# Kernel optimization log

Measured on AMD Instinct MI355X. Metric: run time of the kernel, lower is better.

## Reference

```python
import jax, jax.numpy as jnp
import numpy as np

B, S, DM, H = 4, 2048, 512, 8
HD = DM // H


def setup_inputs() -> dict:
    key = jax.random.key(0)
    ks = jax.random.split(key, 12)
    x = jax.random.normal(ks[0], (B, S, DM), dtype=jnp.float32)
    # causal lower-triangular mask [B, S, S]
    mask = jnp.broadcast_to(jnp.tril(jnp.ones((S, S), dtype=jnp.int32)), (B, S, S))
    # sorted irregular day offsets (trading-day-like), in days
    days_offset = jnp.sort(
        jax.random.uniform(ks[1], (B, S), dtype=jnp.float32) * 3000.0, axis=-1
    )
    scale = 1.0 / np.sqrt(DM)
    Wq = jax.random.normal(ks[2], (DM, DM), dtype=jnp.float32) * scale
    bq = jnp.zeros((DM,), dtype=jnp.float32)
    Wk = jax.random.normal(ks[3], (DM, DM), dtype=jnp.float32) * scale
    bk = jnp.zeros((DM,), dtype=jnp.float32)
    Wv = jax.random.normal(ks[4], (DM, DM), dtype=jnp.float32) * scale
    bv = jnp.zeros((DM,), dtype=jnp.float32)
    Wo = jax.random.normal(ks[5], (DM, DM), dtype=jnp.float32) * scale
    bo = jnp.zeros((DM,), dtype=jnp.float32)
    decay_rate = jnp.float32(0.1)
    return {
        "x": x, "mask": mask, "days_offset": days_offset,
        "Wq": Wq, "bq": bq, "Wk": Wk, "bk": bk,
        "Wv": Wv, "bv": bv, "Wo": Wo, "bo": bo,
        "decay_rate": decay_rate,
    }


def reference(x, mask, days_offset, Wq, bq, Wk, bk, Wv, bv, Wo, bo, decay_rate):
    b, s, _ = x.shape
    # projections (torch Linear: x @ W.T + b), split heads -> [b, h, s, hd]
    def proj(W, bias):
        return (x @ W.T + bias).reshape(b, s, H, HD).transpose(0, 2, 1, 3)
    q, k, v = proj(Wq, bq), proj(Wk, bk), proj(Wv, bv)
    scores = jnp.einsum("bhqd,bhkd->bhqk", q, k) / jnp.sqrt(jnp.float32(HD))
    # temporal decay: exp(-rate * |t_i - t_j|), broadcast over heads
    dist = jnp.abs(days_offset[:, :, None] - days_offset[:, None, :])  # [b,s,s]
    decay = jnp.exp(-decay_rate * dist)
    scores = scores * decay[:, None, :, :]
    scores = jnp.where(mask[:, None, :, :] == 0, -jnp.inf, scores)
    attn = jax.nn.softmax(scores, axis=-1)  # dropout p=0 (eval)
    out = jnp.einsum("bhqk,bhkd->bhqd", attn, v)
    out = out.transpose(0, 2, 1, 3).reshape(b, s, DM)
    return out @ Wo.T + bo
```

## Files before the change

kernel.cpp:

```cpp
#include <hip/hip_runtime.h>
#include <hip/hip_fp16.h>


#define S_LEN 2048
#define DMODEL 512
#define NH 8
#define HD 64

typedef _Float16 half8 __attribute__((ext_vector_type(8)));
typedef _Float16 half4 __attribute__((ext_vector_type(4)));
typedef float floatx4 __attribute__((ext_vector_type(4)));

__device__ __forceinline__ void gload16(const _Float16* g, _Float16* l) {
    __builtin_amdgcn_global_load_lds(
        (const __attribute__((address_space(1))) void*)g,
        (__attribute__((address_space(3))) void*)l, 16, 0, 0);
}

__device__ __forceinline__ half8 cvt8(float4 a, float4 b) {
    half8 h;
    h[0] = (_Float16)a.x; h[1] = (_Float16)a.y; h[2] = (_Float16)a.z; h[3] = (_Float16)a.w;
    h[4] = (_Float16)b.x; h[5] = (_Float16)b.y; h[6] = (_Float16)b.z; h[7] = (_Float16)b.w;
    return h;
}

__device__ __forceinline__ void stage_f32(
    const float* __restrict__ src, _Float16* __restrict__ dstbase,
    int row, int sw, int lane7, int kcol)
{
    const float* p = src + (size_t)row * DMODEL + kcol + sw * 8;
    float4 a = *(const float4*)p;
    float4 b = *(const float4*)(p + 4);
    *(half8*)(dstbase + row * 64 + lane7 * 8) = cvt8(a, b);
}

__global__ __launch_bounds__(256) void qkv_gemm(
    const float* __restrict__ x,
    const float* __restrict__ Wq, const float* __restrict__ Wk, const float* __restrict__ Wv,
    const float* __restrict__ bq, const float* __restrict__ bk, const float* __restrict__ bv,
    _Float16* __restrict__ outh)
{
    __shared__ _Float16 As[2][128 * 64];
    __shared__ _Float16 Ws[2][128 * 64];
    const int t = threadIdx.x;
    const int bm = blockIdx.x, bn = blockIdx.y, z = blockIdx.z;
    const float* Wp = (z == 0) ? Wq : (z == 1) ? Wk : Wv;
    const float* bias = (z == 0) ? bq : (z == 1) ? bk : bv;
    const int w = t >> 6, lane = t & 63, l15 = lane & 15, quad = lane >> 4;
    const int wrow = (w >> 1) * 64, wcol = (w & 1) * 64;
    const int lrow = lane >> 3, lane7 = lane & 7;
    const int sw = lane7 ^ lrow;
    const float* xb = x  + (size_t)(bm * 128) * DMODEL;
    const float* Wb = Wp + (size_t)(bn * 128) * DMODEL;

    auto stage = [&](int kb, int buf) {
        #pragma unroll
        for (int i = 0; i < 4; ++i) {
            int row = w * 32 + i * 8 + lrow;
            stage_f32(xb, As[buf], row, sw, lane7, kb * 64);
            stage_f32(Wb, Ws[buf], row, sw, lane7, kb * 64);
        }
    };

    floatx4 acc[4][4] = {};
    stage(0, 0);
    for (int kb = 0; kb < 8; ++kb) {
        const int buf = kb & 1;
        __syncthreads();
        if (kb < 7) stage(kb + 1, buf ^ 1);
        #pragma unroll
        for (int kk = 0; kk < 2; ++kk) {
            half8 xf[4], wf[4];
            #pragma unroll
            for (int mt = 0; mt < 4; ++mt)
                xf[mt] = *(const half8*)(&As[buf][(wrow + mt * 16 + l15) * 64 + (((quad + 4 * kk) ^ (l15 & 7)) * 8)]);
            #pragma unroll
            for (int nt = 0; nt < 4; ++nt)
                wf[nt] = *(const half8*)(&Ws[buf][(wcol + nt * 16 + l15) * 64 + (((quad + 4 * kk) ^ (l15 & 7)) * 8)]);
            if (z == 2) {
                #pragma unroll
                for (int mt = 0; mt < 4; ++mt)
                    #pragma unroll
                    for (int nt = 0; nt < 4; ++nt)
                        acc[mt][nt] = __builtin_amdgcn_mfma_f32_16x16x32_f16(xf[mt], wf[nt], acc[mt][nt], 0, 0, 0);
            } else {
                #pragma unroll
                for (int nt = 0; nt < 4; ++nt)
                    #pragma unroll
                    for (int mt = 0; mt < 4; ++mt)
                        acc[nt][mt] = __builtin_amdgcn_mfma_f32_16x16x32_f16(wf[nt], xf[mt], acc[nt][mt], 0, 0, 0);
            }
        }
    }

    if (z == 2) {
        #pragma unroll
        for (int mt = 0; mt < 4; ++mt)
            #pragma unroll
            for (int nt = 0; nt < 4; ++nt) {
                int n = bn * 128 + wcol + nt * 16 + l15;
                float bvv = bias[n];
                int m0 = bm * 128 + wrow + mt * 16 + quad * 4;
                int b = m0 >> 11, s0 = m0 & 2047;
                int hh = n >> 6, hd = n & 63;
                half4 hv;
                #pragma unroll
                for (int r = 0; r < 4; ++r) hv[r] = (_Float16)(acc[mt][nt][r] + bvv);
                *(half4*)(outh + (size_t)2 * (8192 * 512) +
                          ((size_t)(b * NH + hh) * HD + hd) * S_LEN + s0) = hv;
            }
    } else {
        #pragma unroll
        for (int nt = 0; nt < 4; ++nt)
            #pragma unroll
            for (int mt = 0; mt < 4; ++mt) {
                int n0 = bn * 128 + wcol + nt * 16 + quad * 4;
                float4 b4 = *(const float4*)(bias + n0);
                int m = bm * 128 + wrow + mt * 16 + l15;
                int b = m >> 11, s = m & 2047;
                int hh = n0 >> 6, hd0 = n0 & 63;
                half4 hv;
                hv[0] = (_Float16)(acc[nt][mt][0] + b4.x);
                hv[1] = (_Float16)(acc[nt][mt][1] + b4.y);
                hv[2] = (_Float16)(acc[nt][mt][2] + b4.z);
                hv[3] = (_Float16)(acc[nt][mt][3] + b4.w);
                *(half4*)(outh + (size_t)z * (8192 * 512) +
                          ((size_t)(b * NH + hh) * S_LEN + s) * HD + hd0) = hv;
            }
    }
}

__global__ __launch_bounds__(256) void out_gemm(
    const _Float16* __restrict__ A, const float* __restrict__ Wo,
    const float* __restrict__ bo, float* __restrict__ outf)
{
    __shared__ _Float16 As[2][64 * 64];
    __shared__ _Float16 Ws[2][128 * 64];
    const int t = threadIdx.x;
    const int bm = blockIdx.x, bn = blockIdx.y;
    const int w = t >> 6, lane = t & 63, l15 = lane & 15, quad = lane >> 4;
    const int wn = w * 32;
    const int lrow = lane >> 3, lane7 = lane & 7;
    const int sw = lane7 ^ lrow;
    const _Float16* Ab = A  + (size_t)(bm * 64) * DMODEL;
    const float*    Wb = Wo + (size_t)(bn * 128) * DMODEL;

    auto stage = [&](int kb, int buf) {
        #pragma unroll
        for (int i = 0; i < 2; ++i) {
            int row = (w * 2 + i) * 8 + lrow;
            gload16(Ab + (size_t)row * DMODEL + kb * 64 + sw * 8, &As[buf][row * 64]);
        }
        #pragma unroll
        for (int i = 0; i < 4; ++i)
            stage_f32(Wb, Ws[buf], w * 32 + i * 8 + lrow, sw, lane7, kb * 64);
    };

    floatx4 acc[2][4] = {};
    stage(0, 0);
    for (int kb = 0; kb < 8; ++kb) {
        const int buf = kb & 1;
        __syncthreads();
        if (kb < 7) stage(kb + 1, buf ^ 1);
        #pragma unroll
        for (int kk = 0; kk < 2; ++kk) {
            half8 wf[2], af[4];
            #pragma unroll
            for (int nt = 0; nt < 2; ++nt)
                wf[nt] = *(const half8*)(&Ws[buf][(wn + nt * 16 + l15) * 64 + (((quad + 4 * kk) ^ (l15 & 7)) * 8)]);
            #pragma unroll
            for (int mt = 0; mt < 4; ++mt)
                af[mt] = *(const half8*)(&As[buf][(mt * 16 + l15) * 64 + (((quad + 4 * kk) ^ (l15 & 7)) * 8)]);
            #pragma unroll
            for (int nt = 0; nt < 2; ++nt)
                #pragma unroll
                for (int mt = 0; mt < 4; ++mt)
                    acc[nt][mt] = __builtin_amdgcn_mfma_f32_16x16x32_f16(wf[nt], af[mt], acc[nt][mt], 0, 0, 0);
        }
    }

    #pragma unroll
    for (int nt = 0; nt < 2; ++nt)
        #pragma unroll
        for (int mt = 0; mt < 4; ++mt) {
            int n0 = bn * 128 + wn + nt * 16 + quad * 4;
            float4 b4 = *(const float4*)(bo + n0);
            int m = bm * 64 + mt * 16 + l15;
            float4 v;
            v.x = acc[nt][mt][0] + b4.x; v.y = acc[nt][mt][1] + b4.y;
            v.z = acc[nt][mt][2] + b4.z; v.w = acc[nt][mt][3] + b4.w;
            *(float4*)(outf + (size_t)m * DMODEL + n0) = v;
        }
}

__global__ __launch_bounds__(512, 2) void attn_k(
    const _Float16* __restrict__ Qh, const _Float16* __restrict__ Kh,
    const _Float16* __restrict__ Vt, const float* __restrict__ days,
    const float* __restrict__ rate_p, _Float16* __restrict__ Ah)
{
    __shared__ float eks_all[2048];
    __shared__ float tk0s[32];
    __shared__ _Float16 Ps[16][16 * 64];

    const int h = blockIdx.x, y = blockIdx.y, b = blockIdx.z;
    const int t = threadIdx.x, w = t >> 6, lane = t & 63;
    const int l15 = lane & 15, quad = lane >> 4, e7 = l15 & 7;
    const float rate = rate_p[0];
    const size_t bhoff = (size_t)(b * NH + h) * (size_t)(S_LEN * HD);
    const _Float16* Qb = Qh + bhoff;
    const _Float16* Kb = Kh + bhoff;
    const _Float16* Vb = Vt + bhoff;
    const float* daysb = days + b * S_LEN;

    {
        int k0 = t * 4;
        float tk0 = daysb[k0 & ~63];
        #pragma unroll
        for (int i = 0; i < 4; ++i) {
            float d = daysb[k0 + i];
            eks_all[k0 + i] = __expf(fminf(rate * (d - tk0), 80.f));
        }
        if (t < 32) tk0s[t] = daysb[t * 64];
    }
    __syncthreads();

    const int wi = w & 3;
    const int j = (w >> 2) ? (15 - y) : y;
    const int s = 4 * j + wi;
    const int q0 = s * 32;
    const int nt = (s >> 1) + 1;

    half8 qf[2][2];
    #pragma unroll
    for (int qc = 0; qc < 2; ++qc)
        #pragma unroll
        for (int kk = 0; kk < 2; ++kk)
            qf[qc][kk] = *(const half8*)(Qb + (size_t)(q0 + qc * 16 + l15) * HD + kk * 32 + quad * 8);

    const int   qg0 = q0 + l15,       qg1 = q0 + 16 + l15;
    const float tq0 = daysb[qg0],     tq1 = daysb[qg1];

    floatx4 oacc[2][4] = {};
    float lacc[2] = {0.f, 0.f};

    half8 kf[4][2];
    half8 vf[4][2];

    auto load_kf = [&](int kt) {
        #pragma unroll
        for (int c = 0; c < 4; ++c)
            #pragma unroll
            for (int kk = 0; kk < 2; ++kk)
                kf[c][kk] = *(const half8*)(Kb + (size_t)(kt * 64 + c * 16 + l15) * HD + kk * 32 + quad * 8);
    };

    auto do_tile = [&](int kt, bool dg, bool pre) {
        #pragma unroll
        for (int s4 = 0; s4 < 4; ++s4)
            #pragma unroll
            for (int kk = 0; kk < 2; ++kk)
                vf[s4][kk] = *(const half8*)(Vb + (size_t)(s4 * 16 + l15) * S_LEN + kt * 64 + kk * 32 + quad * 8);

        floatx4 sc[2][4];
        __builtin_amdgcn_s_setprio(1);
        #pragma unroll
        for (int c = 0; c < 4; ++c) {
            floatx4 z0 = {}, z1 = {};
            z0 = __builtin_amdgcn_mfma_f32_16x16x32_f16(kf[c][0], qf[0][0], z0, 0, 0, 0);
            z1 = __builtin_amdgcn_mfma_f32_16x16x32_f16(kf[c][0], qf[1][0], z1, 0, 0, 0);
            sc[0][c] = __builtin_amdgcn_mfma_f32_16x16x32_f16(kf[c][1], qf[0][1], sc[0][c] = z0, 0, 0, 0);
            sc[1][c] = __builtin_amdgcn_mfma_f32_16x16x32_f16(kf[c][1], qf[1][1], sc[1][c] = z1, 0, 0, 0);
        }
        __builtin_amdgcn_s_setprio(0);

        if (pre) load_kf(kt + 1);

        const float tk0 = tk0s[kt];
        const float eq0 = 0.125f * __expf(-rate * (tq0 - tk0));
        const float eq1 = 0.125f * __expf(-rate * (tq1 - tk0));
        #pragma unroll
        for (int c = 0; c < 4; ++c) {
            floatx4 ek4 = *(const floatx4*)(&eks_all[kt * 64 + c * 16 + quad * 4]);
            #pragma unroll
            for (int qc = 0; qc < 2; ++qc) {
                const float eqv = qc ? eq1 : eq0;
                const int   qg  = qc ? qg1 : qg0;
                float pv[4];
                #pragma unroll
                for (int r = 0; r < 4; ++r) {
                    float p = __expf(sc[qc][c][r] * (eqv * ek4[r]));
                    if (dg && (kt * 64 + c * 16 + quad * 4 + r) > qg) p = 0.f;
                    lacc[qc] += p;
                    pv[r] = p;
                }
                half4 hv;
                hv[0] = (_Float16)pv[0]; hv[1] = (_Float16)pv[1];
                hv[2] = (_Float16)pv[2]; hv[3] = (_Float16)pv[3];
                *(half4*)(&Ps[w * 2 + qc][l15 * 64 + (((2 * c + (quad >> 1)) ^ e7) * 8) + (quad & 1) * 4]) = hv;
            }
        }

        __builtin_amdgcn_s_setprio(1);
        #pragma unroll
        for (int qc = 0; qc < 2; ++qc) {
            half8 pf0 = *(const half8*)(&Ps[w * 2 + qc][l15 * 64 + ((quad ^ e7) * 8)]);
            half8 pf1 = *(const half8*)(&Ps[w * 2 + qc][l15 * 64 + (((4 + quad) ^ e7) * 8)]);
            #pragma unroll
            for (int s4 = 0; s4 < 4; ++s4) {
                oacc[qc][s4] = __builtin_amdgcn_mfma_f32_16x16x32_f16(vf[s4][0], pf0, oacc[qc][s4], 0, 0, 0);
                oacc[qc][s4] = __builtin_amdgcn_mfma_f32_16x16x32_f16(vf[s4][1], pf1, oacc[qc][s4], 0, 0, 0);
            }
        }
        __builtin_amdgcn_s_setprio(0);
    };

    load_kf(0);
    for (int kt = 0; kt < nt - 1; ++kt)
        do_tile(kt, false, true);
    do_tile(nt - 1, true, false);

    #pragma unroll
    for (int qc = 0; qc < 2; ++qc) {
        float l = lacc[qc];
        l += __shfl_xor(l, 16);
        l += __shfl_xor(l, 32);
        float linv = 1.0f / l;
        const int qg = qc ? qg1 : qg0;
        #pragma unroll
        for (int s4 = 0; s4 < 4; ++s4) {
            half4 hv;
            #pragma unroll
            for (int r = 0; r < 4; ++r) hv[r] = (_Float16)(oacc[qc][s4][r] * linv);
            *(half4*)(Ah + ((size_t)(b * S_LEN) + qg) * DMODEL + h * HD + s4 * 16 + quad * 4) = hv;
        }
    }
}

extern "C" void kernel_launch(void* const* d_in, const int* in_sizes, int n_in,
                              void* d_out, int out_size, void* d_ws, size_t ws_size,
                              hipStream_t stream)
{
    const float* x    = (const float*)d_in[0];
    const float* days = (const float*)d_in[2];
    const float* Wq   = (const float*)d_in[3];
    const float* bq   = (const float*)d_in[4];
    const float* Wk   = (const float*)d_in[5];
    const float* bk   = (const float*)d_in[6];
    const float* Wv   = (const float*)d_in[7];
    const float* bv   = (const float*)d_in[8];
    const float* Wo   = (const float*)d_in[9];
    const float* bo   = (const float*)d_in[10];
    const float* rate = (const float*)d_in[11];
    float* out = (float*)d_out;

    _Float16* Qh = (_Float16*)d_ws;
    _Float16* Kh = Qh + 4194304;
    _Float16* Vh = Kh + 4194304;
    _Float16* Ah = Vh + 4194304;

    dim3 g0(64, 4, 3);
    qkv_gemm<<<g0, 256, 0, stream>>>(x, Wq, Wk, Wv, bq, bk, bv, Qh);

    dim3 ga(NH, 8, 4);
    attn_k<<<ga, 512, 0, stream>>>(Qh, Kh, Vh, days, rate, Ah);

    dim3 g1(128, 4, 1);
    out_gemm<<<g1, 256, 0, stream>>>(Ah, Wo, bo, out);
}
```

Before: 230.7 us.

## Restructure attention: LDS-staged K/V tiles, split-K warps, double-buffered pipeline

Rewrites the attention kernel to stage K and V tiles into shared memory with async global-to-LDS loads and double buffering, instead of each warp loading K/V from global memory directly. Each block now covers 64 query rows with 4 warps. Warps split the key tile in halves and reduce partial outputs and softmax sums through LDS at the end. Decay factors are computed per tile rather than precomputed for the whole sequence, and the grid grows to 32 blocks per head with reversed ordering for causal load balance. This trades more barriers and a final cross-warp reduction for shared K/V reuse and software pipelining of the score and PV stages.

Result: faster. 218.2 us (-5.4%).

```diff
diff --git a/kernel.cpp b/kernel.cpp
--- a/kernel.cpp
+++ b/kernel.cpp
@@ -193,43 +193,49 @@
         }
 }
 
-__global__ __launch_bounds__(512, 2) void attn_k(
+__global__ __launch_bounds__(256, 3) void attn_k(
     const _Float16* __restrict__ Qh, const _Float16* __restrict__ Kh,
     const _Float16* __restrict__ Vt, const float* __restrict__ days,
     const float* __restrict__ rate_p, _Float16* __restrict__ Ah)
 {
-    __shared__ float eks_all[2048];
-    __shared__ float tk0s[32];
-    __shared__ _Float16 Ps[16][16 * 64];
-
-    const int h = blockIdx.x, y = blockIdx.y, b = blockIdx.z;
+    __shared__ _Float16 Ks[2][64 * 64];
+    __shared__ _Float16 Vs[2][64 * 64];
+    __shared__ float    eks[2][64];
+    __shared__ float4   PsRaw[1024];
+    __shared__ float    lred[2][2][64];
+
+    _Float16* Ps  = (_Float16*)PsRaw;
+    float*    PsF = (float*)PsRaw;
+
+    const int h = blockIdx.x, b = blockIdx.z;
+    const int j = 31 - blockIdx.y;
     const int t = threadIdx.x, w = t >> 6, lane = t & 63;
     const int l15 = lane & 15, quad = lane >> 4, e7 = l15 & 7;
+    const int qh = w & 1, kh = w >> 1;
     const float rate = rate_p[0];
     const size_t bhoff = (size_t)(b * NH + h) * (size_t)(S_LEN * HD);
     const _Float16* Qb = Qh + bhoff;
     const _Float16* Kb = Kh + bhoff;
     const _Float16* Vb = Vt + bhoff;
     const float* daysb = days + b * S_LEN;
-
-    {
-        int k0 = t * 4;
-        float tk0 = daysb[k0 & ~63];
-        #pragma unroll
-        for (int i = 0; i < 4; ++i) {
-            float d = daysb[k0 + i];
-            eks_all[k0 + i] = __expf(fminf(rate * (d - tk0), 80.f));
-        }
-        if (t < 32) tk0s[t] = daysb[t * 64];
-    }
-    __syncthreads();
-
-    const int wi = w & 3;
-    const int j = (w >> 2) ? (15 - y) : y;
-    const int s = 4 * j + wi;
-    const int q0 = s * 32;
-    const int nt = (s >> 1) + 1;
-
+    const int lrow = lane >> 3, sw = (lane & 7) ^ lrow;
+
+    auto stage = [&](int kt, int buf) {
+        #pragma unroll
+        for (int i = 0; i < 2; ++i) {
+            int grp = w * 2 + i;
+            int row = grp * 8 + lrow;
+            gload16(Kb + (size_t)(kt * 64 + row) * HD + sw * 8, &Ks[buf][grp * 512]);
+            gload16(Vb + (size_t)row * S_LEN + kt * 64 + sw * 8, &Vs[buf][grp * 512]);
+        }
+        if (w == 0) {
+            float tk0 = daysb[kt * 64];
+            float d = daysb[kt * 64 + lane];
+            eks[buf][lane] = __expf(fminf(rate * (d - tk0), 80.f));
+        }
+    };
+
+    const int q0 = j * 64 + qh * 32;
     half8 qf[2][2];
     #pragma unroll
     for (int qc = 0; qc < 2; ++qc)
@@ -237,101 +243,131 @@
         for (int kk = 0; kk < 2; ++kk)
             qf[qc][kk] = *(const half8*)(Qb + (size_t)(q0 + qc * 16 + l15) * HD + kk * 32 + quad * 8);
 
-    const int   qg0 = q0 + l15,       qg1 = q0 + 16 + l15;
-    const float tq0 = daysb[qg0],     tq1 = daysb[qg1];
+    const int   qg[2] = {q0 + l15, q0 + 16 + l15};
+    const float tq[2] = {daysb[qg[0]], daysb[qg[1]]};
 
     floatx4 oacc[2][4] = {};
     float lacc[2] = {0.f, 0.f};
 
-    half8 kf[4][2];
-    half8 vf[4][2];
-
-    auto load_kf = [&](int kt) {
-        #pragma unroll
-        for (int c = 0; c < 4; ++c)
+    floatx4 scA[2][2], scB[2][2];
+    half8  vfA[4], vfB[4];
+    floatx4 ekA[2], ekB[2];
+    float  eqA[2], eqB[2];
+
+    auto load_tile = [&](int kt, int par, floatx4 (&sc)[2][2], half8 (&vf)[4],
+                         floatx4 (&ek)[2], float (&eq)[2]) {
+        half8 kf[2][2];
+        #pragma unroll
+        for (int c = 0; c < 2; ++c) {
+            const int C = kh * 2 + c;
             #pragma unroll
             for (int kk = 0; kk < 2; ++kk)
-                kf[c][kk] = *(const half8*)(Kb + (size_t)(kt * 64 + c * 16 + l15) * HD + kk * 32 + quad * 8);
+                kf[c][kk] = *(const half8*)(&Ks[par][(C * 16 + l15) * 64 + (((quad + 4 * kk) ^ e7) * 8)]);
+        }
+        #pragma unroll
+        for (int qc = 0; qc < 2; ++qc)
+            #pragma unroll
+            for (int c = 0; c < 2; ++c) {
+                floatx4 z = {};
+                z = __builtin_amdgcn_mfma_f32_16x16x32_f16(kf[c][0], qf[qc][0], z, 0, 0, 0);
+                sc[qc][c] = __builtin_amdgcn_mfma_f32_16x16x32_f16(kf[c][1], qf[qc][1], z, 0, 0, 0);
+            }
+        #pragma unroll
+        for (int s4 = 0; s4 < 4; ++s4)
+            vf[s4] = *(const half8*)(&Vs[par][(s4 * 16 + l15) * 64 + (((quad + 4 * kh) ^ e7) * 8)]);
+        const float tk0 = daysb[kt * 64];
+        #pragma unroll
+        for (int qc = 0; qc < 2; ++qc)
+            eq[qc] = 0.125f * __expf(-rate * (tq[qc] - tk0));
+        #pragma unroll
+        for (int c = 0; c < 2; ++c)
+            ek[c] = *(const floatx4*)(&eks[par][kh * 32 + c * 16 + quad * 4]);
     };
 
-    auto do_tile = [&](int kt, bool dg, bool pre) {
-        #pragma unroll
-        for (int s4 = 0; s4 < 4; ++s4)
-            #pragma unroll
-            for (int kk = 0; kk < 2; ++kk)
-                vf[s4][kk] = *(const half8*)(Vb + (size_t)(s4 * 16 + l15) * S_LEN + kt * 64 + kk * 32 + quad * 8);
-
-        floatx4 sc[2][4];
-        __builtin_amdgcn_s_setprio(1);
-        #pragma unroll
-        for (int c = 0; c < 4; ++c) {
-            floatx4 z0 = {}, z1 = {};
-            z0 = __builtin_amdgcn_mfma_f32_16x16x32_f16(kf[c][0], qf[0][0], z0, 0, 0, 0);
-            z1 = __builtin_amdgcn_mfma_f32_16x16x32_f16(kf[c][0], qf[1][0], z1, 0, 0, 0);
-            sc[0][c] = __builtin_amdgcn_mfma_f32_16x16x32_f16(kf[c][1], qf[0][1], sc[0][c] = z0, 0, 0, 0);
-            sc[1][c] = __builtin_amdgcn_mfma_f32_16x16x32_f16(kf[c][1], qf[1][1], sc[1][c] = z1, 0, 0, 0);
-        }
-        __builtin_amdgcn_s_setprio(0);
-
-        if (pre) load_kf(kt + 1);
-
-        const float tk0 = tk0s[kt];
-        const float eq0 = 0.125f * __expf(-rate * (tq0 - tk0));
-        const float eq1 = 0.125f * __expf(-rate * (tq1 - tk0));
-        #pragma unroll
-        for (int c = 0; c < 4; ++c) {
-            floatx4 ek4 = *(const floatx4*)(&eks_all[kt * 64 + c * 16 + quad * 4]);
-            #pragma unroll
-            for (int qc = 0; qc < 2; ++qc) {
-                const float eqv = qc ? eq1 : eq0;
-                const int   qg  = qc ? qg1 : qg0;
+    auto softmax_pv = [&](floatx4 (&sc)[2][2], half8 (&vf)[4],
+                          floatx4 (&ek)[2], float (&eq)[2], bool dg, int kt) {
+        #pragma unroll
+        for (int qc = 0; qc < 2; ++qc)
+            #pragma unroll
+            for (int c = 0; c < 2; ++c) {
                 float pv[4];
                 #pragma unroll
                 for (int r = 0; r < 4; ++r) {
-                    float p = __expf(sc[qc][c][r] * (eqv * ek4[r]));
-                    if (dg && (kt * 64 + c * 16 + quad * 4 + r) > qg) p = 0.f;
+                    float p = __expf(sc[qc][c][r] * (eq[qc] * ek[c][r]));
+                    if (dg && (kt * 64 + kh * 32 + c * 16 + quad * 4 + r) > qg[qc]) p = 0.f;
                     lacc[qc] += p;
                     pv[r] = p;
                 }
                 half4 hv;
                 hv[0] = (_Float16)pv[0]; hv[1] = (_Float16)pv[1];
                 hv[2] = (_Float16)pv[2]; hv[3] = (_Float16)pv[3];
-                *(half4*)(&Ps[w * 2 + qc][l15 * 64 + (((2 * c + (quad >> 1)) ^ e7) * 8) + (quad & 1) * 4]) = hv;
-            }
-        }
-
-        __builtin_amdgcn_s_setprio(1);
+                *(half4*)(&Ps[(w * 2 + qc) * 1024 + l15 * 64 +
+                              (((kh * 4 + 2 * c + (quad >> 1)) ^ e7) * 8) + (quad & 1) * 4]) = hv;
+            }
         #pragma unroll
         for (int qc = 0; qc < 2; ++qc) {
-            half8 pf0 = *(const half8*)(&Ps[w * 2 + qc][l15 * 64 + ((quad ^ e7) * 8)]);
-            half8 pf1 = *(const half8*)(&Ps[w * 2 + qc][l15 * 64 + (((4 + quad) ^ e7) * 8)]);
+            half8 pf = *(const half8*)(&Ps[(w * 2 + qc) * 1024 + l15 * 64 + (((quad + 4 * kh) ^ e7) * 8)]);
+            #pragma unroll
+            for (int s4 = 0; s4 < 4; ++s4)
+                oacc[qc][s4] = __builtin_amdgcn_mfma_f32_16x16x32_f16(vf[s4], pf, oacc[qc][s4], 0, 0, 0);
+        }
+    };
+
+    stage(0, 0);
+    __syncthreads();
+    if (j > 0) stage(1, 1);
+    load_tile(0, 0, scA, vfA, ekA, eqA);
+
+    int kt = 1;
+    for (; kt + 1 <= j; kt += 2) {
+        const int p1 = kt & 1;
+        __syncthreads();
+        if (kt < j) stage(kt + 1, p1 ^ 1);
+        load_tile(kt, p1, scB, vfB, ekB, eqB);
+        softmax_pv(scA, vfA, ekA, eqA, false, kt - 1);
+        const int p2 = p1 ^ 1;
+        __syncthreads();
+        if (kt + 1 < j) stage(kt + 2, p2 ^ 1);
+        load_tile(kt + 1, p2, scA, vfA, ekA, eqA);
+        softmax_pv(scB, vfB, ekB, eqB, false, kt);
+    }
+    if (kt <= j) {
+        const int p1 = kt & 1;
+        __syncthreads();
+        load_tile(kt, p1, scB, vfB, ekB, eqB);
+        softmax_pv(scA, vfA, ekA, eqA, false, kt - 1);
+        softmax_pv(scB, vfB, ekB, eqB, true, j);
+    } else {
+        softmax_pv(scA, vfA, ekA, eqA, true, j);
+    }
+
+    __syncthreads();
+    if (w >= 2) {
+        #pragma unroll
+        for (int qc = 0; qc < 2; ++qc) {
+            #pragma unroll
+            for (int s4 = 0; s4 < 4; ++s4)
+                *(floatx4*)(&PsF[(((w & 1) * 2 + qc) * 4 + s4) * 256 + lane * 4]) = oacc[qc][s4];
+            lred[w & 1][qc][lane] = lacc[qc];
+        }
+    }
+    __syncthreads();
+    if (w < 2) {
+        #pragma unroll
+        for (int qc = 0; qc < 2; ++qc) {
+            float l = lacc[qc] + lred[w][qc][lane];
+            l += __shfl_xor(l, 16);
+            l += __shfl_xor(l, 32);
+            const float linv = 1.0f / l;
             #pragma unroll
             for (int s4 = 0; s4 < 4; ++s4) {
-                oacc[qc][s4] = __builtin_amdgcn_mfma_f32_16x16x32_f16(vf[s4][0], pf0, oacc[qc][s4], 0, 0, 0);
-                oacc[qc][s4] = __builtin_amdgcn_mfma_f32_16x16x32_f16(vf[s4][1], pf1, oacc[qc][s4], 0, 0, 0);
-            }
-        }
-        __builtin_amdgcn_s_setprio(0);
-    };
-
-    load_kf(0);
-    for (int kt = 0; kt < nt - 1; ++kt)
-        do_tile(kt, false, true);
-    do_tile(nt - 1, true, false);
-
-    #pragma unroll
-    for (int qc = 0; qc < 2; ++qc) {
-        float l = lacc[qc];
-        l += __shfl_xor(l, 16);
-        l += __shfl_xor(l, 32);
-        float linv = 1.0f / l;
-        const int qg = qc ? qg1 : qg0;
-        #pragma unroll
-        for (int s4 = 0; s4 < 4; ++s4) {
-            half4 hv;
-            #pragma unroll
-            for (int r = 0; r < 4; ++r) hv[r] = (_Float16)(oacc[qc][s4][r] * linv);
-            *(half4*)(Ah + ((size_t)(b * S_LEN) + qg) * DMODEL + h * HD + s4 * 16 + quad * 4) = hv;
+                floatx4 o = oacc[qc][s4] +
+                    *(const floatx4*)(&PsF[((w * 2 + qc) * 4 + s4) * 256 + lane * 4]);
+                half4 hv;
+                #pragma unroll
+                for (int r = 0; r < 4; ++r) hv[r] = (_Float16)(o[r] * linv);
+                *(half4*)(Ah + ((size_t)(b * S_LEN) + qg[qc]) * DMODEL + h * HD + s4 * 16 + quad * 4) = hv;
+            }
         }
     }
 }
@@ -361,9 +397,9 @@
     dim3 g0(64, 4, 3);
     qkv_gemm<<<g0, 256, 0, stream>>>(x, Wq, Wk, Wv, bq, bk, bv, Qh);
 
-    dim3 ga(NH, 8, 4);
-    attn_k<<<ga, 512, 0, stream>>>(Qh, Kh, Vh, days, rate, Ah);
+    dim3 ga(NH, 32, 4);
+    attn_k<<<ga, 256, 0, stream>>>(Qh, Kh, Vh, days, rate, Ah);
 
     dim3 g1(128, 4, 1);
-    out_gemm<<<g1, 256, 0, stream>>>(Ah, Wo, bo, out);
-}
+    out_gemm<<<g1, 4 * 64, 0, stream>>>(Ah, Wo, bo, out);
+}
```
